# Performance work log

Measured on AMD Instinct MI355X. Metric: run time of the kernel, lower is better.

The kernel has to match this reference:

```python
import jax, jax.numpy as jnp
import numpy as np

B, N, D = 4, 2048, 1024
H = 16
DH = D // H


def setup_inputs() -> dict:
    key = jax.random.key(0)
    ks = jax.random.split(key, 9)
    s_in = 1.0 / np.sqrt(D)
    x = jax.random.normal(ks[0], (B, N, D), dtype=jnp.float32)
    Wq = jax.random.uniform(ks[1], (D, D), jnp.float32, -s_in, s_in)
    bq = jax.random.uniform(ks[2], (D,), jnp.float32, -s_in, s_in)
    Wk = jax.random.uniform(ks[3], (D, D), jnp.float32, -s_in, s_in)
    bk = jax.random.uniform(ks[4], (D,), jnp.float32, -s_in, s_in)
    Wv = jax.random.uniform(ks[5], (D, D), jnp.float32, -s_in, s_in)
    bv = jax.random.uniform(ks[6], (D,), jnp.float32, -s_in, s_in)
    Wo = jax.random.uniform(ks[7], (D, D), jnp.float32, -s_in, s_in)
    bo = jax.random.uniform(ks[8], (D,), jnp.float32, -s_in, s_in)
    return {"x": x, "Wq": Wq, "bq": bq, "Wk": Wk, "bk": bk,
            "Wv": Wv, "bv": bv, "Wo": Wo, "bo": bo}


def reference(x, Wq, bq, Wk, bk, Wv, bv, Wo, bo):
    b, n, d = x.shape
    q = (x @ Wq + bq).reshape(b, n, H, DH)  # (b, n, h, dh)
    k = (x @ Wk + bk).reshape(b, n, H, DH)
    v = (x @ Wv + bv).reshape(b, n, H, DH)
    scale = 1.0 / jnp.sqrt(jnp.asarray(DH, x.dtype))
    scores = jnp.einsum("bqhd,bkhd->bhqk", q, k) * scale  # (b, h, n, n)
    # valid = arange(1..n) per query => causal mask: key index < valid[q] = q+1
    causal = jnp.arange(n)[None, :] <= jnp.arange(n)[:, None]  # (n_q, n_k)
    scores = jnp.where(causal[None, None, :, :], scores, -jnp.inf)
    weights = jax.nn.softmax(scores, axis=-1)
    out = jnp.einsum("bhqk,bkhd->bqhd", weights, v).reshape(b, n, d)
    return out @ Wo + bo
```

## Files before the change

kernel.cpp:

```cpp
#include <hip/hip_runtime.h>
#include <hip/hip_bf16.h>
#include <math.h>

namespace {
constexpr int B_ = 4, N_ = 2048, D_ = 1024, H_ = 16, DH_ = 64;
constexpr int M_ = B_ * N_;
}

typedef __bf16 bf16x8 __attribute__((ext_vector_type(8)));
typedef __bf16 bf16x4 __attribute__((ext_vector_type(4)));
typedef float  f32x4  __attribute__((ext_vector_type(4)));

__device__ inline void async_copy16(const void* g, void* l) {
    __builtin_amdgcn_global_load_lds(
        (const __attribute__((address_space(1))) unsigned int*)g,
        (__attribute__((address_space(3))) unsigned int*)l, 16, 0, 0);
}

__device__ inline float fast_exp2(float x) {
#if __has_builtin(__builtin_amdgcn_exp2f)
    return __builtin_amdgcn_exp2f(x);
#else
    return exp2f(x);
#endif
}

__device__ inline int swz(int row, int c) {
    return c ^ (row & 3) ^ ((row >> 2) & 3);
}

__global__ __launch_bounds__(256) void cast_xw(
        const float* __restrict__ x, __bf16* __restrict__ xb,
        const float* __restrict__ Wq, const float* __restrict__ Wk,
        const float* __restrict__ Wv, const float* __restrict__ Wo,
        __bf16* __restrict__ wqkvt, __bf16* __restrict__ wot)
{
    __shared__ float t[64][65];
    const int bid = blockIdx.x;
    const int tid = threadIdx.x;
    if (bid < 4096) {
        const size_t i = ((size_t)bid * 256 + tid) * 8;
        const float4 a = *reinterpret_cast<const float4*>(x + i);
        const float4 b = *reinterpret_cast<const float4*>(x + i + 4);
        bf16x8 o;
        o[0] = (__bf16)a.x; o[1] = (__bf16)a.y; o[2] = (__bf16)a.z; o[3] = (__bf16)a.w;
        o[4] = (__bf16)b.x; o[5] = (__bf16)b.y; o[6] = (__bf16)b.z; o[7] = (__bf16)b.w;
        *reinterpret_cast<bf16x8*>(xb + i) = o;
    } else {
        const int b2 = bid - 4096;
        const int bx = b2 & 15, by = (b2 >> 4) & 15, z = b2 >> 8;
        const float* W = (z == 0) ? Wq : (z == 1) ? Wk : (z == 2) ? Wv : Wo;
        __bf16* dst = (z < 3) ? (wqkvt + (size_t)z * D_ * D_) : wot;
        const int k0 = bx * 64, n0 = by * 64;
        #pragma unroll
        for (int p = 0; p < 16; ++p) {
            const int idx = p * 256 + tid;
            const int r = idx >> 6, c = idx & 63;
            t[r][c] = W[(size_t)(k0 + r) * D_ + n0 + c];
        }
        __syncthreads();
        #pragma unroll
        for (int p = 0; p < 16; ++p) {
            const int idx = p * 256 + tid;
            const int r = idx >> 6, c = idx & 63;
            dst[(size_t)(n0 + r) * D_ + k0 + c] = (__bf16)t[c][r];
        }
    }
}

__global__ __launch_bounds__(256) void qkv_mfma(
        const __bf16* __restrict__ A, const __bf16* __restrict__ Bt,
        const float* __restrict__ bq, const float* __restrict__ bk,
        const float* __restrict__ bv,
        __bf16* __restrict__ qo, __bf16* __restrict__ ko, __bf16* __restrict__ vo)
{
    __shared__ __align__(16) __bf16 As[128 * 32];
    __shared__ __align__(16) __bf16 Bs[128 * 32];
    const int tid = threadIdx.x;
    const int w = tid >> 6, lane = tid & 63;
    const int l15 = lane & 15, quad = lane >> 4;
    const int tm = blockIdx.x * 128;
    const int tn = blockIdx.y * 128;

    f32x4 acc[4][4] = {};

    for (int k0 = 0; k0 < D_; k0 += 32) {
        __syncthreads();
        #pragma unroll
        for (int it = 0; it < 2; ++it) {
            const int c = it * 256 + tid;
            const int r = c >> 2, pc = c & 3;
            const int lc = swz(r, pc);
            async_copy16(A + (size_t)(tm + r) * D_ + k0 + lc * 8, As + c * 8);
            async_copy16(Bt + (size_t)(tn + r) * D_ + k0 + lc * 8, Bs + c * 8);
        }
        __syncthreads();

        bf16x8 af[4], bfr[4];
        #pragma unroll
        for (int t = 0; t < 4; ++t) {
            const int row = (w >> 1) * 64 + t * 16 + l15;
            af[t] = *reinterpret_cast<const bf16x8*>(
                As + (row * 4 + swz(row, quad)) * 8);
            const int col = (w & 1) * 64 + t * 16 + l15;
            bfr[t] = *reinterpret_cast<const bf16x8*>(
                Bs + (col * 4 + swz(col, quad)) * 8);
        }
        #pragma unroll
        for (int mt = 0; mt < 4; ++mt)
            #pragma unroll
            for (int nt = 0; nt < 4; ++nt)
                acc[mt][nt] = __builtin_amdgcn_mfma_f32_16x16x32_bf16(
                    af[mt], bfr[nt], acc[mt][nt], 0, 0, 0);
    }

    const int z = blockIdx.y >> 3;
    const float* bias = (z == 0) ? bq : (z == 1) ? bk : bv;
    const int col0 = (blockIdx.y & 7) * 128 + (w & 1) * 64;
    const int h = col0 >> 6;
    float bcol[4];
    #pragma unroll
    for (int nt = 0; nt < 4; ++nt) bcol[nt] = bias[col0 + nt * 16 + l15];
    const int gr0 = tm + (w >> 1) * 64;

    if (z < 2) {
        __bf16* dst = (z == 0) ? qo : ko;
        const float sc = (z == 0) ? 0.125f * 1.44269504f : 1.0f;
        #pragma unroll
        for (int mt = 0; mt < 4; ++mt)
            #pragma unroll
            for (int i = 0; i < 4; ++i) {
                const int gr = gr0 + mt * 16 + quad * 4 + i;
                const int b = gr >> 11, tok = gr & (N_ - 1);
                __bf16* row = dst + ((size_t)(b * H_ + h) * N_ + tok) * DH_;
                #pragma unroll
                for (int nt = 0; nt < 4; ++nt)
                    row[nt * 16 + l15] = (__bf16)((acc[mt][nt][i] + bcol[nt]) * sc);
            }
    } else {
        #pragma unroll
        for (int mt = 0; mt < 4; ++mt) {
            const int gr = gr0 + mt * 16 + quad * 4;
            const int b = gr >> 11, tok = gr & (N_ - 1);
            #pragma unroll
            for (int nt = 0; nt < 4; ++nt) {
                const int dh = nt * 16 + l15;
                bf16x4 pv;
                #pragma unroll
                for (int i = 0; i < 4; ++i)
                    pv[i] = (__bf16)(acc[mt][nt][i] + bcol[nt]);
                *reinterpret_cast<bf16x4*>(
                    vo + ((size_t)(b * H_ + h) * DH_ + dh) * N_ + tok) = pv;
            }
        }
    }
}

__global__ __launch_bounds__(256) void out_mfma(
        const __bf16* __restrict__ A, const __bf16* __restrict__ Bt,
        const float* __restrict__ bias, float* __restrict__ out)
{
    __shared__ __align__(16) __bf16 As[128 * 32];
    __shared__ __align__(16) __bf16 Bs[128 * 32];
    const int tid = threadIdx.x;
    const int w = tid >> 6, lane = tid & 63;
    const int l15 = lane & 15, quad = lane >> 4;
    const int tm = blockIdx.x * 128;
    const int tn = blockIdx.y * 128;

    f32x4 acc[4][4] = {};

    for (int k0 = 0; k0 < D_; k0 += 32) {
        __syncthreads();
        #pragma unroll
        for (int it = 0; it < 2; ++it) {
            const int c = it * 256 + tid;
            const int r = c >> 2, pc = c & 3;
            const int lc = swz(r, pc);
            async_copy16(A + (size_t)(tm + r) * D_ + k0 + lc * 8, As + c * 8);
            async_copy16(Bt + (size_t)(tn + r) * D_ + k0 + lc * 8, Bs + c * 8);
        }
        __syncthreads();

        bf16x8 af[4], bfr[4];
        #pragma unroll
        for (int t = 0; t < 4; ++t) {
            const int row = (w >> 1) * 64 + t * 16 + l15;
            af[t] = *reinterpret_cast<const bf16x8*>(
                As + (row * 4 + swz(row, quad)) * 8);
            const int col = (w & 1) * 64 + t * 16 + l15;
            bfr[t] = *reinterpret_cast<const bf16x8*>(
                Bs + (col * 4 + swz(col, quad)) * 8);
        }
        #pragma unroll
        for (int mt = 0; mt < 4; ++mt)
            #pragma unroll
            for (int nt = 0; nt < 4; ++nt)
                acc[mt][nt] = __builtin_amdgcn_mfma_f32_16x16x32_bf16(
                    af[mt], bfr[nt], acc[mt][nt], 0, 0, 0);
    }

    const int col0 = tn + (w & 1) * 64;
    float bcol[4];
    #pragma unroll
    for (int nt = 0; nt < 4; ++nt) bcol[nt] = bias[col0 + nt * 16 + l15];
    const int gr0 = tm + (w >> 1) * 64;
    #pragma unroll
    for (int mt = 0; mt < 4; ++mt)
        #pragma unroll
        for (int i = 0; i < 4; ++i) {
            const int gr = gr0 + mt * 16 + quad * 4 + i;
            float* row = out + (size_t)gr * D_;
            #pragma unroll
            for (int nt = 0; nt < 4; ++nt)
                row[col0 + nt * 16 + l15] = acc[mt][nt][i] + bcol[nt];
        }
}

__global__ __launch_bounds__(256, 3) void attn(
        const __bf16* __restrict__ Q, const __bf16* __restrict__ K,
        const __bf16* __restrict__ Vt, __bf16* __restrict__ ctx)
{
    const int blk = blockIdx.x;
    const int bh = blk & 63;
    const int pp = blk >> 6;
    const int tid = threadIdx.x;
    const int w = tid >> 6, lane = tid & 63;
    const int l15 = lane & 15, quad = lane >> 4;

    __shared__ __align__(16) __bf16 Ks[2][64 * 64];
    __shared__ __align__(16) __bf16 Vs[2][64 * 64];
    __shared__ __align__(16) __bf16 Ps[4][2][16 * 72];

    const __bf16* Kg = K + (size_t)bh * N_ * DH_;
    const __bf16* Vg = Vt + (size_t)bh * DH_ * N_;
    const int b = bh >> 4, h = bh & 15;
    const int sr = lane >> 3;
    const int sc = lane & 7;

    auto stage = [&](int kb) {
        const int sl = kb & 1;
        #pragma unroll
        for (int j = 0; j < 2; ++j) {
            const int r = j * 32 + w * 8 + sr;
            const int cl = sc ^ (r & 7);
            async_copy16(Kg + (size_t)(kb * 64 + r) * DH_ + cl * 8,
                         &Ks[sl][(j * 256 + tid) * 8]);
            async_copy16(Vg + (size_t)r * N_ + kb * 64 + cl * 8,
                         &Vs[sl][(j * 256 + tid) * 8]);
        }
    };

    #pragma unroll 1
    for (int half = 0; half < 2; ++half) {
        const int qb = half ? pp : 15 - pp;
        const int qt0 = qb * 128;
        const int nkb = 2 * qb + 2;

        bf16x8 bqf[2][2];
        #pragma unroll
        for (int qc = 0; qc < 2; ++qc) {
            const size_t base =
                ((size_t)bh * N_ + qt0 + w * 32 + qc * 16 + l15) * DH_;
            bqf[qc][0] = *reinterpret_cast<const bf16x8*>(Q + base + quad * 8);
            bqf[qc][1] = *reinterpret_cast<const bf16x8*>(Q + base + 32 + quad * 8);
        }

        f32x4 acc[2][4] = {};
        float l_lane[2] = {0.f, 0.f};

        stage(0);
        asm volatile("s_waitcnt vmcnt(0)" ::: "memory");
        __builtin_amdgcn_s_barrier();

        #pragma unroll 1
        for (int kb = 0; kb < nkb; ++kb) {
            const int sl = kb & 1;
            if (kb + 1 < nkb) stage(kb + 1);
            const __bf16* Ksl = Ks[sl];
            const __bf16* Vsl = Vs[sl];

            f32x4 st[2][4];
            __builtin_amdgcn_s_setprio(1);
            #pragma unroll
            for (int ct = 0; ct < 4; ++ct) {
                const int row = ct * 16 + l15;
                const bf16x8 ka0 = *reinterpret_cast<const bf16x8*>(
                    &Ksl[(row * 8 + (quad ^ (row & 7))) * 8]);
                const bf16x8 ka1 = *reinterpret_cast<const bf16x8*>(
                    &Ksl[(row * 8 + ((quad + 4) ^ (row & 7))) * 8]);
                #pragma unroll
                for (int qc = 0; qc < 2; ++qc) {
                    f32x4 t = {};
                    t = __builtin_amdgcn_mfma_f32_16x16x32_bf16(ka0, bqf[qc][0], t, 0, 0, 0);
                    t = __builtin_amdgcn_mfma_f32_16x16x32_bf16(ka1, bqf[qc][1], t, 0, 0, 0);
                    st[qc][ct] = t;
                }
            }
            __builtin_amdgcn_s_setprio(0);
            if (kb >= 2 * qb) {
                #pragma unroll
                for (int qc = 0; qc < 2; ++qc) {
                    const int q_glob = qt0 + w * 32 + qc * 16 + l15;
                    #pragma unroll
                    for (int ct = 0; ct < 4; ++ct)
                        #pragma unroll
                        for (int i = 0; i < 4; ++i) {
                            const int k_glob = kb * 64 + ct * 16 + quad * 4 + i;
                            if (k_glob > q_glob) st[qc][ct][i] = -INFINITY;
                        }
                }
            }

            #pragma unroll
            for (int qc = 0; qc < 2; ++qc) {
                float rs = 0.f;
                #pragma unroll
                for (int ct = 0; ct < 4; ++ct) {
                    bf16x4 pk;
                    #pragma unroll
                    for (int i = 0; i < 4; ++i) {
                        const float p = fast_exp2(st[qc][ct][i]);
                        rs += p;
                        pk[i] = (__bf16)p;
                    }
                    *reinterpret_cast<bf16x4*>(
                        &Ps[w][qc][l15 * 72 + ct * 16 + quad * 4]) = pk;
                }
                l_lane[qc] += rs;
            }

            bf16x8 pa0[2], pa1[2];
            #pragma unroll
            for (int qc = 0; qc < 2; ++qc) {
                pa0[qc] = *reinterpret_cast<const bf16x8*>(
                    &Ps[w][qc][l15 * 72 + quad * 8]);
                pa1[qc] = *reinterpret_cast<const bf16x8*>(
                    &Ps[w][qc][l15 * 72 + 32 + quad * 8]);
            }
            __builtin_amdgcn_s_setprio(1);
            #pragma unroll
            for (int ct = 0; ct < 4; ++ct) {
                const int row = ct * 16 + l15;
                const bf16x8 vb0 = *reinterpret_cast<const bf16x8*>(
                    &Vsl[(row * 8 + (quad ^ (row & 7))) * 8]);
                const bf16x8 vb1 = *reinterpret_cast<const bf16x8*>(
                    &Vsl[(row * 8 + ((quad + 4) ^ (row & 7))) * 8]);
                #pragma unroll
                for (int qc = 0; qc < 2; ++qc) {
                    f32x4 t = acc[qc][ct];
                    t = __builtin_amdgcn_mfma_f32_16x16x32_bf16(pa0[qc], vb0, t, 0, 0, 0);
                    t = __builtin_amdgcn_mfma_f32_16x16x32_bf16(pa1[qc], vb1, t, 0, 0, 0);
                    acc[qc][ct] = t;
                }
            }
            __builtin_amdgcn_s_setprio(0);

            asm volatile("s_waitcnt vmcnt(0)" ::: "memory");
            __builtin_amdgcn_s_barrier();
        }

        #pragma unroll
        for (int qc = 0; qc < 2; ++qc) {
            float r = l_lane[qc];
            r += __shfl_xor(r, 16);
            r += __shfl_xor(r, 32);
            const float linv = 1.0f / r;
            float lT[4];
            #pragma unroll
            for (int i = 0; i < 4; ++i) lT[i] = __shfl(linv, quad * 4 + i);
            #pragma unroll
            for (int i = 0; i < 4; ++i) {
                const int row = qt0 + w * 32 + qc * 16 + quad * 4 + i;
                __bf16* dst = ctx + ((size_t)b * N_ + row) * D_ + h * DH_;
                #pragma unroll
                for (int ct = 0; ct < 4; ++ct)
                    dst[ct * 16 + l15] = (__bf16)(acc[qc][ct][i] * lT[i]);
            }
        }
    }
}

extern "C" void kernel_launch(void* const* d_in, const int* in_sizes, int n_in,
                              void* d_out, int out_size, void* d_ws, size_t ws_size,
                              hipStream_t stream) {
    const float* x  = (const float*)d_in[0];
    const float* Wq = (const float*)d_in[1];
    const float* bq = (const float*)d_in[2];
    const float* Wk = (const float*)d_in[3];
    const float* bk = (const float*)d_in[4];
    const float* Wv = (const float*)d_in[5];
    const float* bv = (const float*)d_in[6];
    const float* Wo = (const float*)d_in[7];
    const float* bo = (const float*)d_in[8];
    float* out = (float*)d_out;

    __bf16* xb    = (__bf16*)d_ws;
    __bf16* wqkvt = xb + (size_t)M_ * D_;
    __bf16* wot   = wqkvt + (size_t)3 * D_ * D_;
    __bf16* q     = wot + (size_t)D_ * D_;
    __bf16* k     = q + (size_t)M_ * D_;
    __bf16* vt    = k + (size_t)M_ * D_;
    __bf16* ctx   = vt + (size_t)M_ * D_;

    cast_xw<<<dim3(4096 + 1024), 256, 0, stream>>>(
        x, xb, Wq, Wk, Wv, Wo, wqkvt, wot);
    qkv_mfma<<<dim3(M_ / 128, 3 * D_ / 128), 256, 0, stream>>>(
        xb, wqkvt, bq, bk, bv, q, k, vt);
    attn<<<dim3(512), 256, 0, stream>>>(q, k, vt, ctx);
    out_mfma<<<dim3(M_ / 128, D_ / 128), 256, 0, stream>>>(ctx, wot, bo, out);
}
```

Baseline: 244.6 us.

## Process long and short causal query blocks in one shared K/V pass

The attention kernel used to run the long and short query blocks of each balanced pair one after the other, streaming K/V tiles twice. It now keeps both query tiles' fragments and accumulators live and walks the K/V blocks once, computing the short tile alongside the long one for the first nkbS blocks. This halves K/V global traffic and staging for the overlapping range. In exchange it roughly doubles register pressure, so the launch-bounds occupancy hint drops from 3 to 2 blocks per SM.

```diff
diff --git a/kernel.cpp b/kernel.cpp
--- a/kernel.cpp
+++ b/kernel.cpp
@@ -217,7 +217,7 @@
         }
 }
 
-__global__ __launch_bounds__(256, 3) void attn(
+__global__ __launch_bounds__(256, 2) void attn(
         const __bf16* __restrict__ Q, const __bf16* __restrict__ K,
         const __bf16* __restrict__ Vt, __bf16* __restrict__ ctx)
 {
@@ -238,6 +238,10 @@
     const int sr = lane >> 3;
     const int sc = lane & 7;
 
+    const int qbL = 15 - pp, qbS = pp;
+    const int qt0L = qbL * 128, qt0S = qbS * 128;
+    const int nkbL = 2 * qbL + 2, nkbS = 2 * qbS + 2;
+
     auto stage = [&](int kb) {
         const int sl = kb & 1;
         #pragma unroll
@@ -251,118 +255,123 @@
         }
     };
 
+    bf16x8 bqfL[2][2], bqfS[2][2];
+    #pragma unroll
+    for (int qc = 0; qc < 2; ++qc) {
+        const size_t baseL =
+            ((size_t)bh * N_ + qt0L + w * 32 + qc * 16 + l15) * DH_;
+        bqfL[qc][0] = *reinterpret_cast<const bf16x8*>(Q + baseL + quad * 8);
+        bqfL[qc][1] = *reinterpret_cast<const bf16x8*>(Q + baseL + 32 + quad * 8);
+        const size_t baseS =
+            ((size_t)bh * N_ + qt0S + w * 32 + qc * 16 + l15) * DH_;
+        bqfS[qc][0] = *reinterpret_cast<const bf16x8*>(Q + baseS + quad * 8);
+        bqfS[qc][1] = *reinterpret_cast<const bf16x8*>(Q + baseS + 32 + quad * 8);
+    }
+
+    f32x4 accL[2][4] = {}, accS[2][4] = {};
+    float llL[2] = {0.f, 0.f}, llS[2] = {0.f, 0.f};
+
+    auto tile_qb = [&](const __bf16* Ksl, const __bf16* Vsl,
+                       bf16x8 (&bqf)[2][2], f32x4 (&acc)[2][4],
+                       float (&ll)[2], int qt0, int diag0, int kb) {
+        f32x4 st[2][4];
+        __builtin_amdgcn_s_setprio(1);
+        #pragma unroll
+        for (int ct = 0; ct < 4; ++ct) {
+            const int row = ct * 16 + l15;
+            const bf16x8 ka0 = *reinterpret_cast<const bf16x8*>(
+                &Ksl[(row * 8 + (quad ^ (row & 7))) * 8]);
+            const bf16x8 ka1 = *reinterpret_cast<const bf16x8*>(
+                &Ksl[(row * 8 + ((quad + 4) ^ (row & 7))) * 8]);
+            #pragma unroll
+            for (int qc = 0; qc < 2; ++qc) {
+                f32x4 t = {};
+                t = __builtin_amdgcn_mfma_f32_16x16x32_bf16(ka0, bqf[qc][0], t, 0, 0, 0);
+                t = __builtin_amdgcn_mfma_f32_16x16x32_bf16(ka1, bqf[qc][1], t, 0, 0, 0);
+                st[qc][ct] = t;
+            }
+        }
+        __builtin_amdgcn_s_setprio(0);
+        if (kb >= diag0) {
+            #pragma unroll
+            for (int qc = 0; qc < 2; ++qc) {
+                const int q_glob = qt0 + w * 32 + qc * 16 + l15;
+                #pragma unroll
+                for (int ct = 0; ct < 4; ++ct)
+                    #pragma unroll
+                    for (int i = 0; i < 4; ++i) {
+                        const int k_glob = kb * 64 + ct * 16 + quad * 4 + i;
+                        if (k_glob > q_glob) st[qc][ct][i] = -INFINITY;
+                    }
+            }
+        }
+        #pragma unroll
+        for (int qc = 0; qc < 2; ++qc) {
+            float rs = 0.f;
+            #pragma unroll
+            for (int ct = 0; ct < 4; ++ct) {
+                bf16x4 pk;
+                #pragma unroll
+                for (int i = 0; i < 4; ++i) {
+                    const float p = fast_exp2(st[qc][ct][i]);
+                    rs += p;
+                    pk[i] = (__bf16)p;
+                }
+                *reinterpret_cast<bf16x4*>(
+                    &Ps[w][qc][l15 * 72 + ct * 16 + quad * 4]) = pk;
+            }
+            ll[qc] += rs;
+        }
+        bf16x8 pa0[2], pa1[2];
+        #pragma unroll
+        for (int qc = 0; qc < 2; ++qc) {
+            pa0[qc] = *reinterpret_cast<const bf16x8*>(
+                &Ps[w][qc][l15 * 72 + quad * 8]);
+            pa1[qc] = *reinterpret_cast<const bf16x8*>(
+                &Ps[w][qc][l15 * 72 + 32 + quad * 8]);
+        }
+        __builtin_amdgcn_s_setprio(1);
+        #pragma unroll
+        for (int ct = 0; ct < 4; ++ct) {
+            const int row = ct * 16 + l15;
+            const bf16x8 vb0 = *reinterpret_cast<const bf16x8*>(
+                &Vsl[(row * 8 + (quad ^ (row & 7))) * 8]);
+            const bf16x8 vb1 = *reinterpret_cast<const bf16x8*>(
+                &Vsl[(row * 8 + ((quad + 4) ^ (row & 7))) * 8]);
+            #pragma unroll
+            for (int qc = 0; qc < 2; ++qc) {
+                f32x4 t = acc[qc][ct];
+                t = __builtin_amdgcn_mfma_f32_16x16x32_bf16(pa0[qc], vb0, t, 0, 0, 0);
+                t = __builtin_amdgcn_mfma_f32_16x16x32_bf16(pa1[qc], vb1, t, 0, 0, 0);
+                acc[qc][ct] = t;
+            }
+        }
+        __builtin_amdgcn_s_setprio(0);
+    };
+
+    stage(0);
+    asm volatile("s_waitcnt vmcnt(0)" ::: "memory");
+    __builtin_amdgcn_s_barrier();
+
     #pragma unroll 1
-    for (int half = 0; half < 2; ++half) {
-        const int qb = half ? pp : 15 - pp;
-        const int qt0 = qb * 128;
-        const int nkb = 2 * qb + 2;
-
-        bf16x8 bqf[2][2];
-        #pragma unroll
-        for (int qc = 0; qc < 2; ++qc) {
-            const size_t base =
-                ((size_t)bh * N_ + qt0 + w * 32 + qc * 16 + l15) * DH_;
-            bqf[qc][0] = *reinterpret_cast<const bf16x8*>(Q + base + quad * 8);
-            bqf[qc][1] = *reinterpret_cast<const bf16x8*>(Q + base + 32 + quad * 8);
-        }
-
-        f32x4 acc[2][4] = {};
-        float l_lane[2] = {0.f, 0.f};
-
-        stage(0);
+    for (int kb = 0; kb < nkbL; ++kb) {
+        const int sl = kb & 1;
+        if (kb + 1 < nkbL) stage(kb + 1);
+        const __bf16* Ksl = Ks[sl];
+        const __bf16* Vsl = Vs[sl];
+
+        tile_qb(Ksl, Vsl, bqfL, accL, llL, qt0L, 2 * qbL, kb);
+        if (kb < nkbS)
+            tile_qb(Ksl, Vsl, bqfS, accS, llS, qt0S, 2 * qbS, kb);
+
         asm volatile("s_waitcnt vmcnt(0)" ::: "memory");
         __builtin_amdgcn_s_barrier();
-
-        #pragma unroll 1
-        for (int kb = 0; kb < nkb; ++kb) {
-            const int sl = kb & 1;
-            if (kb + 1 < nkb) stage(kb + 1);
-            const __bf16* Ksl = Ks[sl];
-            const __bf16* Vsl = Vs[sl];
-
-            f32x4 st[2][4];
-            __builtin_amdgcn_s_setprio(1);
-            #pragma unroll
-            for (int ct = 0; ct < 4; ++ct) {
-                const int row = ct * 16 + l15;
-                const bf16x8 ka0 = *reinterpret_cast<const bf16x8*>(
-                    &Ksl[(row * 8 + (quad ^ (row & 7))) * 8]);
-                const bf16x8 ka1 = *reinterpret_cast<const bf16x8*>(
-                    &Ksl[(row * 8 + ((quad + 4) ^ (row & 7))) * 8]);
-                #pragma unroll
-                for (int qc = 0; qc < 2; ++qc) {
-                    f32x4 t = {};
-                    t = __builtin_amdgcn_mfma_f32_16x16x32_bf16(ka0, bqf[qc][0], t, 0, 0, 0);
-                    t = __builtin_amdgcn_mfma_f32_16x16x32_bf16(ka1, bqf[qc][1], t, 0, 0, 0);
-                    st[qc][ct] = t;
-                }
-            }
-            __builtin_amdgcn_s_setprio(0);
-            if (kb >= 2 * qb) {
-                #pragma unroll
-                for (int qc = 0; qc < 2; ++qc) {
-                    const int q_glob = qt0 + w * 32 + qc * 16 + l15;
-                    #pragma unroll
-                    for (int ct = 0; ct < 4; ++ct)
-                        #pragma unroll
-                        for (int i = 0; i < 4; ++i) {
-                            const int k_glob = kb * 64 + ct * 16 + quad * 4 + i;
-                            if (k_glob > q_glob) st[qc][ct][i] = -INFINITY;
-                        }
-                }
-            }
-
-            #pragma unroll
-            for (int qc = 0; qc < 2; ++qc) {
-                float rs = 0.f;
-                #pragma unroll
-                for (int ct = 0; ct < 4; ++ct) {
-                    bf16x4 pk;
-                    #pragma unroll
-                    for (int i = 0; i < 4; ++i) {
-                        const float p = fast_exp2(st[qc][ct][i]);
-                        rs += p;
-                        pk[i] = (__bf16)p;
-                    }
-                    *reinterpret_cast<bf16x4*>(
-                        &Ps[w][qc][l15 * 72 + ct * 16 + quad * 4]) = pk;
-                }
-                l_lane[qc] += rs;
-            }
-
-            bf16x8 pa0[2], pa1[2];
-            #pragma unroll
-            for (int qc = 0; qc < 2; ++qc) {
-                pa0[qc] = *reinterpret_cast<const bf16x8*>(
-                    &Ps[w][qc][l15 * 72 + quad * 8]);
-                pa1[qc] = *reinterpret_cast<const bf16x8*>(
-                    &Ps[w][qc][l15 * 72 + 32 + quad * 8]);
-            }
-            __builtin_amdgcn_s_setprio(1);
-            #pragma unroll
-            for (int ct = 0; ct < 4; ++ct) {
-                const int row = ct * 16 + l15;
-                const bf16x8 vb0 = *reinterpret_cast<const bf16x8*>(
-                    &Vsl[(row * 8 + (quad ^ (row & 7))) * 8]);
-                const bf16x8 vb1 = *reinterpret_cast<const bf16x8*>(
-                    &Vsl[(row * 8 + ((quad + 4) ^ (row & 7))) * 8]);
-                #pragma unroll
-                for (int qc = 0; qc < 2; ++qc) {
-                    f32x4 t = acc[qc][ct];
-                    t = __builtin_amdgcn_mfma_f32_16x16x32_bf16(pa0[qc], vb0, t, 0, 0, 0);
-                    t = __builtin_amdgcn_mfma_f32_16x16x32_bf16(pa1[qc], vb1, t, 0, 0, 0);
-                    acc[qc][ct] = t;
-                }
-            }
-            __builtin_amdgcn_s_setprio(0);
-
-            asm volatile("s_waitcnt vmcnt(0)" ::: "memory");
-            __builtin_amdgcn_s_barrier();
-        }
-
+    }
+
+    auto epilogue = [&](f32x4 (&acc)[2][4], float (&ll)[2], int qt0) {
         #pragma unroll
         for (int qc = 0; qc < 2; ++qc) {
-            float r = l_lane[qc];
+            float r = ll[qc];
             r += __shfl_xor(r, 16);
             r += __shfl_xor(r, 32);
             const float linv = 1.0f / r;
@@ -378,7 +387,9 @@
                     dst[ct * 16 + l15] = (__bf16)(acc[qc][ct][i] * lT[i]);
             }
         }
-    }
+    };
+    epilogue(accL, llL, qt0L);
+    epilogue(accS, llS, qt0S);
 }
 
 extern "C" void kernel_launch(void* const* d_in, const int* in_sizes, int n_in,
```

Result: no change. 243.0 us, median of 4 (-0.7%).
